# Performance work log

Hardware: AMD Instinct MI355X
Metric: run time of the kernel (lower is better)

The kernel has to match this reference:

```python
import jax, jax.numpy as jnp
import numpy as np

N = 100_000
E = 1_600_000
F_IN, D1, D2, D_EMB = 64, 32, 64, 64
NUM_GRAPHS = 16
BN_EPS = 1e-5


def _glorot(key, shape):
    fan_in, fan_out = shape[0], shape[1]
    lim = (6.0 / (fan_in + fan_out)) ** 0.5
    return jax.random.uniform(key, shape, jnp.float32, -lim, lim)


def setup_inputs() -> dict:
    key = jax.random.key(0)
    ks = jax.random.split(key, 12)
    x = jax.random.normal(ks[0], (N, F_IN), jnp.float32)
    edge_index = jax.random.randint(ks[1], (2, E), 0, N, jnp.int64)
    batch = jnp.sort(jax.random.randint(ks[2], (N,), 0, NUM_GRAPHS, jnp.int64))
    return {
        "x": x,
        "edge_index": edge_index,
        "batch": batch,
        "num_graphs": NUM_GRAPHS,
        "num_nodes": N,
        "W1a": _glorot(ks[3], (F_IN, D1)), "b1a": jnp.zeros((D1,), jnp.float32),
        "W1b": _glorot(ks[4], (D1, D2)), "b1b": jnp.zeros((D2,), jnp.float32),
        "g1": jnp.ones((D2,), jnp.float32), "be1": jnp.zeros((D2,), jnp.float32),
        "W2a": _glorot(ks[5], (D2, D2)), "b2a": jnp.zeros((D2,), jnp.float32),
        "W2b": _glorot(ks[6], (D2, D_EMB)), "b2b": jnp.zeros((D_EMB,), jnp.float32),
        "g2": jnp.ones((D_EMB,), jnp.float32), "be2": jnp.zeros((D_EMB,), jnp.float32),
    }


def _batchnorm_train(h, gamma, beta):
    mean = jnp.mean(h, axis=0)
    var = jnp.mean(jnp.square(h - mean), axis=0)  # biased var, as torch BN uses for normalization
    return (h - mean) * jax.lax.rsqrt(var + BN_EPS) * gamma + beta


def _gin_aggregate(x, src, dst, valid, n_nodes):
    # sum_{j in N(i)} x_j over valid edges only (masked scatter-add)
    msg = x[src] * valid[:, None]  # [E, D]
    return jax.ops.segment_sum(msg, dst, num_segments=n_nodes)


def reference(x, edge_index, batch, num_graphs, num_nodes,
              W1a, b1a, W1b, b1b, g1, be1,
              W2a, b2a, W2b, b2b, g2, be2):
    n_edges = edge_index.shape[1]
    per = n_edges // num_graphs
    # edge_mask: per-edge threshold g * num_nodes / num_graphs applied to both rows
    thresh = jnp.repeat(jnp.arange(num_graphs), per).astype(jnp.float32) * (num_nodes / num_graphs)
    valid = jnp.all(edge_index.astype(jnp.float32) - thresh[None, :] >= 0.0, axis=0)
    valid = valid.astype(x.dtype)
    src, dst = edge_index[0], edge_index[1]

    # GINConv 1 (eps=0): nn1(x + aggr)
    h = x + _gin_aggregate(x, src, dst, valid, num_nodes)
    h = jax.nn.relu(h @ W1a + b1a) @ W1b + b1b
    h = jax.nn.relu(h)
    h = _batchnorm_train(h, g1, be1)

    # GINConv 2
    h = h + _gin_aggregate(h, src, dst, valid, num_nodes)
    h = jax.nn.relu(h @ W2a + b2a) @ W2b + b2b
    h = jax.nn.relu(h)
    h = _batchnorm_train(h, g2, be2)

    # global_mean_pool
    sums = jax.ops.segment_sum(h, batch, num_segments=num_graphs)
    counts = jax.ops.segment_sum(jnp.ones((h.shape[0],), h.dtype), batch, num_segments=num_graphs)
    return sums / jnp.maximum(counts, 1.0)[:, None]
```

## Files before the change

kernel.cpp:

```cpp
#include <hip/hip_runtime.h>
#include <hip/hip_fp16.h>

#define NG 16
#define D 64
#define SLOT 32
#define NPB 128
#define INH 72

union HF4 { float4 f4; __half2 h2[4]; };
union HF2 { float2 f2; __half2 h2[2]; };

typedef _Float16 half4_t __attribute__((ext_vector_type(4)));
typedef float float4_t __attribute__((ext_vector_type(4)));

__device__ __forceinline__ float2 f2fma(float2 a, float2 b, float2 c) {
  return make_float2(fmaf(a.x, b.x, c.x), fmaf(a.y, b.y, c.y));
}

__device__ __forceinline__ void load16(const float4* __restrict__ feat4, int N,
                                       int q8, int4 a, int4 b, int4 c, int4 d,
                                       HF4* u) {
  int ix[16] = {a.x, a.y, a.z, a.w, b.x, b.y, b.z, b.w,
                c.x, c.y, c.z, c.w, d.x, d.y, d.z, d.w};
#pragma unroll
  for (int i = 0; i < 16; i++)
    u[i].f4 = feat4[(size_t)min(ix[i], N) * 8 + q8];
}

__device__ __forceinline__ void acc16(const HF4* u, float2* acc) {
#pragma unroll
  for (int i = 0; i < 16; i++) {
#pragma unroll
    for (int c = 0; c < 4; c++) {
      acc[c].x = fmaf(__low2float(u[i].h2[c]), 1.0f, acc[c].x);
      acc[c].y = fmaf(__high2float(u[i].h2[c]), 1.0f, acc[c].y);
    }
  }
}

__global__ void prep_kernel(const float* __restrict__ x,
                            float2* __restrict__ xh, int n4,
                            float4* __restrict__ xz, float4* __restrict__ hz,
                            const int* __restrict__ ei,
                            int* __restrict__ fill, int* __restrict__ col,
                            int E, int per, int tmul) {
  int t = blockIdx.x * 256 + threadIdx.x;
  if (blockIdx.x == 0 && threadIdx.x < 16) {
    float4 z = make_float4(0.f, 0.f, 0.f, 0.f);
    if (threadIdx.x < 8) xz[threadIdx.x] = z;
    else hz[threadIdx.x - 8] = z;
  }
  if (t < n4) {
    float4 v = ((const float4*)x)[t];
    HF2 u;
    u.h2[0] = __floats2half2_rn(v.x, v.y);
    u.h2[1] = __floats2half2_rn(v.z, v.w);
    xh[t] = u.f2;
  }
  if (t < E) {
    int src = ei[t];
    int dst = ei[E + t];
    int thr = (t / per) * tmul;
    if (src >= thr && dst >= thr) {
      int k = atomicAdd(&fill[dst], 1);
      if (k < SLOT) col[dst * SLOT + k] = src;
    }
  }
}

template <int MID, bool FOLD_BN, int EPI>
__global__ __launch_bounds__(512, 2) void fused_layer_kernel(
    const float4* __restrict__ feat4,
    const int* __restrict__ col, const int* __restrict__ deg,
    const float* __restrict__ bn_sum, const float* __restrict__ bn_sq,
    const float* __restrict__ bn_gamma, const float* __restrict__ bn_beta,
    float invN,
    const float* __restrict__ Wa, const float* __restrict__ ba,
    const float* __restrict__ Wb, const float* __restrict__ bb,
    float2* __restrict__ out2,
    const int* __restrict__ batch,
    float* __restrict__ st_sum,
    float* __restrict__ st_sq,
    float* __restrict__ cnt,
    int N) {
  constexpr int CT = MID / 16;

  __shared__ __align__(16) __half s_h[NPB * INH];
  __shared__ __align__(16) __half s_wa[MID * 64];
  __shared__ __align__(16) __half s_wb[64 * MID];
  __shared__ __align__(16) float s_ba[MID];
  __shared__ __align__(16) float s_bb[D];
  __shared__ float s_bna[FOLD_BN ? D : 1];
  __shared__ float s_bnb[FOLD_BN ? D : 1];
  __shared__ int s_cnt[2];

  int tid = threadIdx.x;
  int base = blockIdx.x * NPB;

  {
    constexpr int WA_SLOTS = MID * 16;
    constexpr int WB_SLOTS = MID * 16;
    for (int g = tid; g < WA_SLOTS + WB_SLOTS; g += 512) {
      half4_t v;
      if (g < WA_SLOTS) {
        int l = g & 63, kt = (g >> 6) & 3, ct = g >> 8;
        int k0 = kt * 16 + ((l >> 4) << 2);
        int c = ct * 16 + (l & 15);
#pragma unroll
        for (int i = 0; i < 4; i++) v[i] = (_Float16)Wa[(k0 + i) * MID + c];
        *(half4_t*)&s_wa[g * 4] = v;
      } else {
        int g2 = g - WA_SLOTS;
        int l = g2 & 63;
        int kt = (g2 >> 6) & (CT - 1);
        int ot = g2 >> (6 + (CT == 4 ? 2 : 1));
        int k0 = kt * 16 + ((l >> 4) << 2);
        int o = ot * 16 + (l & 15);
#pragma unroll
        for (int i = 0; i < 4; i++) v[i] = (_Float16)Wb[(k0 + i) * D + o];
        *(half4_t*)&s_wb[g2 * 4] = v;
      }
    }
  }
  if (tid < MID) s_ba[tid] = ba[tid];
  if (tid < D) s_bb[tid] = bb[tid];
  if (FOLD_BN && tid < D) {
    float mean = bn_sum[tid] * invN;
    float var = bn_sq[tid] * invN - mean * mean;
    float av = bn_gamma[tid] * rsqrtf(var + 1e-5f);
    s_bna[tid] = av;
    s_bnb[tid] = bn_beta[tid] - mean * av;
  }
  if (EPI == 2 && tid < 2) s_cnt[tid] = 0;
  __syncthreads();

  {
    int q8 = tid & 7;
#pragma unroll
    for (int s0 = 0; s0 < 2; s0++) {
      int slot = (tid >> 3) + 64 * s0;
      int node = base + slot;
      float2 acc[4];
      if (node < N) {
        int d = min(deg[node], SLOT);
        const int4* cp = (const int4*)(col + (size_t)node * SLOT);
        {
          HF4 s; s.f4 = feat4[(size_t)node * 8 + q8];
#pragma unroll
          for (int i = 0; i < 4; i++) acc[i] = __half22float2(s.h2[i]);
        }
        HF4 u[16];
        load16(feat4, N, q8, cp[0], cp[1], cp[2], cp[3], u);
        acc16(u, acc);
        if (__any(d > 16)) {
          load16(feat4, N, q8, cp[4], cp[5], cp[6], cp[7], u);
          acc16(u, acc);
        }
        if (FOLD_BN) {
          float dp = (float)(d + 1);
          int c0 = q8 * 8;
#pragma unroll
          for (int c = 0; c < 4; c++) {
            float2 a2 = *(const float2*)&s_bna[c0 + 2 * c];
            float2 b2 = *(const float2*)&s_bnb[c0 + 2 * c];
            acc[c] = f2fma(a2, acc[c], make_float2(dp * b2.x, dp * b2.y));
          }
        }
      } else {
#pragma unroll
        for (int i = 0; i < 4; i++) acc[i] = make_float2(0.f, 0.f);
      }
      HF4 o;
#pragma unroll
      for (int c = 0; c < 4; c++)
        o.h2[c] = __floats2half2_rn(acc[c].x, acc[c].y);
      *(float4*)&s_h[slot * INH + q8 * 8] = o.f4;
    }
  }
  __syncthreads();

  int w = tid >> 6;
  int l = tid & 63;
  int lg = l >> 4;
  int ln = l & 15;
  int nodeB = base + w * 16 + ln;

  half4_t hb[4];
#pragma unroll
  for (int kt = 0; kt < 4; kt++)
    hb[kt] = *(const half4_t*)&s_h[(w * 16 + ln) * INH + kt * 16 + lg * 4];

  float4_t c1[CT];
#pragma unroll
  for (int ct = 0; ct < CT; ct++) {
    c1[ct] = *(const float4_t*)&s_ba[ct * 16 + lg * 4];
#pragma unroll
    for (int kt = 0; kt < 4; kt++) {
      half4_t a = *(const half4_t*)&s_wa[((ct * 4 + kt) * 64 + l) * 4];
      c1[ct] = __builtin_amdgcn_mfma_f32_16x16x16f16(a, hb[kt], c1[ct], 0, 0, 0);
    }
  }
  half4_t mb[CT];
#pragma unroll
  for (int ct = 0; ct < CT; ct++) {
#pragma unroll
    for (int r = 0; r < 4; r++) mb[ct][r] = (_Float16)fmaxf(c1[ct][r], 0.f);
  }
  float4_t o4[4];
#pragma unroll
  for (int ot = 0; ot < 4; ot++) {
    o4[ot] = *(const float4_t*)&s_bb[ot * 16 + lg * 4];
#pragma unroll
    for (int kt = 0; kt < CT; kt++) {
      half4_t a = *(const half4_t*)&s_wb[((ot * CT + kt) * 64 + l) * 4];
      o4[ot] = __builtin_amdgcn_mfma_f32_16x16x16f16(a, mb[kt], o4[ot], 0, 0, 0);
    }
#pragma unroll
    for (int r = 0; r < 4; r++) o4[ot][r] = fmaxf(o4[ot][r], 0.f);
  }

  float* red = (float*)s_h;

  if (EPI == 1) {
    bool val = nodeB < N;
    if (val) {
#pragma unroll
      for (int ot = 0; ot < 4; ot++) {
        HF2 u;
        u.h2[0] = __floats2half2_rn(o4[ot][0], o4[ot][1]);
        u.h2[1] = __floats2half2_rn(o4[ot][2], o4[ot][3]);
        out2[(size_t)nodeB * 16 + ot * 4 + lg] = u.f2;
      }
    }
    float vm = val ? 1.f : 0.f;
#pragma unroll
    for (int ot = 0; ot < 4; ot++) {
      float4_t s, q;
#pragma unroll
      for (int r = 0; r < 4; r++) {
        float x = vm * o4[ot][r];
        s[r] = x; q[r] = x * o4[ot][r];
      }
#pragma unroll
      for (int m = 1; m < 16; m <<= 1) {
#pragma unroll
        for (int r = 0; r < 4; r++) {
          s[r] += __shfl_xor(s[r], m);
          q[r] += __shfl_xor(q[r], m);
        }
      }
      if (ln == 0) {
        *(float4_t*)&red[w * 576 + ot * 16 + lg * 4] = s;
        *(float4_t*)&red[w * 576 + 64 + ot * 16 + lg * 4] = q;
      }
    }
    __syncthreads();
    if (tid < D) {
      float s = 0.f, q = 0.f;
#pragma unroll
      for (int ww = 0; ww < 8; ww++) {
        s += red[ww * 576 + tid];
        q += red[ww * 576 + 64 + tid];
      }
      atomicAdd(&st_sum[tid], s);
      atomicAdd(&st_sq[tid], q);
    }
  }

  if (EPI == 2) {
    bool val = nodeB < N;
    int bl = val ? batch[nodeB] : -1;
    int g_lo = batch[base];
    int g_hi = batch[min(base + NPB - 1, N - 1)];
    float vm = val ? 1.f : 0.f;
    float wlo = (bl == g_lo) ? 1.f : 0.f;
    unsigned long long mlo = __ballot(lg == 0 && bl == g_lo);
    unsigned long long mhi = __ballot(lg == 0 && val && bl != g_lo);
    if (l == 0) {
      atomicAdd(&s_cnt[0], (int)__popcll(mlo));
      atomicAdd(&s_cnt[1], (int)__popcll(mhi));
    }
#pragma unroll
    for (int ot = 0; ot < 4; ot++) {
      float4_t sl, st, sq;
#pragma unroll
      for (int r = 0; r < 4; r++) {
        float x = vm * o4[ot][r];
        sl[r] = wlo * x;
        st[r] = x;
        sq[r] = x * o4[ot][r];
      }
#pragma unroll
      for (int m = 1; m < 16; m <<= 1) {
#pragma unroll
        for (int r = 0; r < 4; r++) {
          sl[r] += __shfl_xor(sl[r], m);
          st[r] += __shfl_xor(st[r], m);
          sq[r] += __shfl_xor(sq[r], m);
        }
      }
      if (ln == 0) {
        *(float4_t*)&red[w * 576 + ot * 16 + lg * 4] = sl;
        float4_t sh;
#pragma unroll
        for (int r = 0; r < 4; r++) sh[r] = st[r] - sl[r];
        *(float4_t*)&red[w * 576 + 64 + ot * 16 + lg * 4] = sh;
        *(float4_t*)&red[w * 576 + 128 + ot * 16 + lg * 4] = sq;
      }
    }
    __syncthreads();
    if (tid < D) {
      float sl = 0.f, sh = 0.f, sq = 0.f;
#pragma unroll
      for (int ww = 0; ww < 8; ww++) {
        sl += red[ww * 576 + tid];
        sh += red[ww * 576 + 64 + tid];
        sq += red[ww * 576 + 128 + tid];
      }
      atomicAdd(&st_sum[g_lo * D + tid], sl);
      if (g_hi != g_lo) atomicAdd(&st_sum[g_hi * D + tid], sh);
      atomicAdd(&st_sq[tid], sq);
    }
    if (tid == 0) {
      atomicAdd(&cnt[g_lo], (float)s_cnt[0]);
      if (g_hi != g_lo) atomicAdd(&cnt[g_hi], (float)s_cnt[1]);
    }
  }
}

__global__ void final_kernel(const float* __restrict__ pool,
                             const float* __restrict__ cnt,
                             const float* __restrict__ sq,
                             const float* __restrict__ gamma,
                             const float* __restrict__ beta,
                             float invN, float* __restrict__ out) {
  int c = threadIdx.x;
  float s = 0.f;
#pragma unroll
  for (int g = 0; g < NG; g++) s += pool[g * D + c];
  float mean = s * invN;
  float var = sq[c] * invN - mean * mean;
  float a = gamma[c] * rsqrtf(var + 1e-5f);
  float b = beta[c] - mean * a;
#pragma unroll
  for (int g = 0; g < NG; g++) {
    float n = cnt[g];
    out[g * D + c] = (a * pool[g * D + c] + n * b) / fmaxf(n, 1.f);
  }
}

extern "C" void kernel_launch(void* const* d_in, const int* in_sizes, int n_in,
                              void* d_out, int out_size, void* d_ws, size_t ws_size,
                              hipStream_t stream) {
  const float* x   = (const float*)d_in[0];
  const int* ei    = (const int*)d_in[1];
  const int* batch = (const int*)d_in[2];
  const float* W1a = (const float*)d_in[5];
  const float* b1a = (const float*)d_in[6];
  const float* W1b = (const float*)d_in[7];
  const float* b1b = (const float*)d_in[8];
  const float* g1  = (const float*)d_in[9];
  const float* be1 = (const float*)d_in[10];
  const float* W2a = (const float*)d_in[11];
  const float* b2a = (const float*)d_in[12];
  const float* W2b = (const float*)d_in[13];
  const float* b2b = (const float*)d_in[14];
  const float* g2  = (const float*)d_in[15];
  const float* be2 = (const float*)d_in[16];

  int N = in_sizes[0] / D;
  int E = in_sizes[1] / 2;
  int per = E / NG;
  int tmul = N / NG;
  float invN = 1.f / (float)N;

  float* ws = (float*)d_ws;
  size_t ndh = (size_t)(N + 1) * D / 2;
  float* h1h = ws;
  float* xh  = ws + ndh;
  int*   col = (int*)(ws + 2 * ndh);
  float* stats = ws + 2 * ndh + (size_t)N * SLOT;
  float* sum1 = stats;
  float* sq1  = stats + 64;
  float* pool = stats + 128;
  float* cnt  = stats + 128 + NG * D;
  float* sq2  = stats + 144 + NG * D;
  int*   fill = (int*)(stats + 208 + NG * D);

  hipMemsetAsync(stats, 0, (208 + NG * D + N) * sizeof(float), stream);
  hipMemsetAsync(col, 0x7F, (size_t)N * SLOT * sizeof(int), stream);

  int n4 = N * D / 4;
  int pgrid = (max(n4, E) + 255) / 256;
  prep_kernel<<<pgrid, 256, 0, stream>>>(
      x, (float2*)xh, n4,
      (float4*)(xh + (size_t)N * D / 2),
      (float4*)(h1h + (size_t)N * D / 2),
      ei, fill, col, E, per, tmul);

  int fblocks = (N + NPB - 1) / NPB;

  fused_layer_kernel<32, false, 1><<<fblocks, 512, 0, stream>>>(
      (const float4*)xh, col, fill, nullptr, nullptr, nullptr, nullptr, invN,
      W1a, b1a, W1b, b1b, (float2*)h1h, nullptr, sum1, sq1, nullptr, N);

  fused_layer_kernel<64, true, 2><<<fblocks, 512, 0, stream>>>(
      (const float4*)h1h, col, fill, sum1, sq1, g1, be1, invN,
      W2a, b2a, W2b, b2b, nullptr, batch, pool, sq2, cnt, N);

  final_kernel<<<1, 64, 0, stream>>>(pool, cnt, sq2, g2, be2, invN, (float*)d_out);
}
```

Measured before the change: 222.6 us.

## Sort nodes by degree within block and skip padded neighbor gathers in chunks

Each block builds a degree histogram and prefix scan in shared memory so the nodes of a block are processed in ascending-degree order. Wavefronts therefore see similar degrees, and neighbor gathers are issued in chunks of four that are skipped when no lane in the wave needs them. This replaces the old fixed 16-neighbor gather, which always loaded padded slots. It adds two extra barriers, shared atomics and a scan per block, and output rows are remapped through the permutation.

```diff
diff --git a/kernel.cpp b/kernel.cpp
--- a/kernel.cpp
+++ b/kernel.cpp
@@ -17,19 +17,16 @@
   return make_float2(fmaf(a.x, b.x, c.x), fmaf(a.y, b.y, c.y));
 }
 
-__device__ __forceinline__ void load16(const float4* __restrict__ feat4, int N,
-                                       int q8, int4 a, int4 b, int4 c, int4 d,
-                                       HF4* u) {
-  int ix[16] = {a.x, a.y, a.z, a.w, b.x, b.y, b.z, b.w,
-                c.x, c.y, c.z, c.w, d.x, d.y, d.z, d.w};
-#pragma unroll
-  for (int i = 0; i < 16; i++)
-    u[i].f4 = feat4[(size_t)min(ix[i], N) * 8 + q8];
-}
-
-__device__ __forceinline__ void acc16(const HF4* u, float2* acc) {
-#pragma unroll
-  for (int i = 0; i < 16; i++) {
+__device__ __forceinline__ void load4(const float4* __restrict__ feat4, int N,
+                                      int q8, int4 c, HF4* u) {
+  u[0].f4 = feat4[(size_t)min(c.x, N) * 8 + q8];
+  u[1].f4 = feat4[(size_t)min(c.y, N) * 8 + q8];
+  u[2].f4 = feat4[(size_t)min(c.z, N) * 8 + q8];
+  u[3].f4 = feat4[(size_t)min(c.w, N) * 8 + q8];
+}
+__device__ __forceinline__ void acc4(const HF4* u, float2* acc) {
+#pragma unroll
+  for (int i = 0; i < 4; i++) {
 #pragma unroll
     for (int c = 0; c < 4; c++) {
       acc[c].x = fmaf(__low2float(u[i].h2[c]), 1.0f, acc[c].x);
@@ -93,9 +90,38 @@
   __shared__ float s_bna[FOLD_BN ? D : 1];
   __shared__ float s_bnb[FOLD_BN ? D : 1];
   __shared__ int s_cnt[2];
+  __shared__ int s_pd[NPB];
+  __shared__ int s_hist[SLOT + 2];
 
   int tid = threadIdx.x;
   int base = blockIdx.x * NPB;
+
+  int ld = 0;
+  if (tid < NPB) {
+    int node = base + tid;
+    ld = (node < N) ? min(deg[node], SLOT) : 0;
+  }
+  if (tid >= NPB && tid < NPB + SLOT + 2) s_hist[tid - NPB] = 0;
+  if (EPI == 2 && tid < 2) s_cnt[tid] = 0;
+  __syncthreads();
+  if (tid < NPB) atomicAdd(&s_hist[ld], 1);
+  __syncthreads();
+  if (tid < 64) {
+    int b = tid;
+    int v = (b <= SLOT) ? s_hist[b] : 0;
+    int sum = v;
+#pragma unroll
+    for (int m = 1; m < 64; m <<= 1) {
+      int t2 = __shfl_up(sum, m, 64);
+      if (tid >= m) sum += t2;
+    }
+    if (b <= SLOT) s_hist[b] = sum - v;
+  }
+  __syncthreads();
+  if (tid < NPB) {
+    int k = atomicAdd(&s_hist[ld], 1);
+    s_pd[k] = tid | (ld << 8);
+  }
 
   {
     constexpr int WA_SLOTS = MID * 16;
@@ -131,7 +157,6 @@
     s_bna[tid] = av;
     s_bnb[tid] = bn_beta[tid] - mean * av;
   }
-  if (EPI == 2 && tid < 2) s_cnt[tid] = 0;
   __syncthreads();
 
   {
@@ -139,36 +164,54 @@
 #pragma unroll
     for (int s0 = 0; s0 < 2; s0++) {
       int slot = (tid >> 3) + 64 * s0;
-      int node = base + slot;
+      int pd = s_pd[slot];
+      int loc = pd & 255;
+      int d = pd >> 8;
+      int node = base + loc;
+      int an = min(node, N - 1);
+      const int4* cp = (const int4*)(col + (size_t)an * SLOT);
+      bool a0 = __any(d > 0), a1 = __any(d > 4);
+      bool a2 = __any(d > 8), a3 = __any(d > 12);
+      int4 c0, c1, c2, c3;
+      if (a0) c0 = cp[0];
+      if (a1) c1 = cp[1];
+      if (a2) c2 = cp[2];
+      if (a3) c3 = cp[3];
+      HF4 self; self.f4 = feat4[(size_t)min(node, N) * 8 + q8];
+      HF4 u[16];
+      if (a0) load4(feat4, N, q8, c0, u + 0);
+      if (a1) load4(feat4, N, q8, c1, u + 4);
+      if (a2) load4(feat4, N, q8, c2, u + 8);
+      if (a3) load4(feat4, N, q8, c3, u + 12);
       float2 acc[4];
-      if (node < N) {
-        int d = min(deg[node], SLOT);
-        const int4* cp = (const int4*)(col + (size_t)node * SLOT);
-        {
-          HF4 s; s.f4 = feat4[(size_t)node * 8 + q8];
-#pragma unroll
-          for (int i = 0; i < 4; i++) acc[i] = __half22float2(s.h2[i]);
+#pragma unroll
+      for (int c = 0; c < 4; c++) acc[c] = __half22float2(self.h2[c]);
+      if (a0) acc4(u + 0, acc);
+      if (a1) acc4(u + 4, acc);
+      if (a2) acc4(u + 8, acc);
+      if (a3) acc4(u + 12, acc);
+      if (__any(d > 16)) {
+        int4 c4 = cp[4], c5 = cp[5], c6 = cp[6], c7 = cp[7];
+        load4(feat4, N, q8, c4, u + 0);
+        load4(feat4, N, q8, c5, u + 4);
+        load4(feat4, N, q8, c6, u + 8);
+        load4(feat4, N, q8, c7, u + 12);
+        acc4(u + 0, acc); acc4(u + 4, acc);
+        acc4(u + 8, acc); acc4(u + 12, acc);
+      }
+      if (FOLD_BN) {
+        float dp = (float)(d + 1);
+        int c0f = q8 * 8;
+#pragma unroll
+        for (int c = 0; c < 4; c++) {
+          float2 a2f = *(const float2*)&s_bna[c0f + 2 * c];
+          float2 b2f = *(const float2*)&s_bnb[c0f + 2 * c];
+          acc[c] = f2fma(a2f, acc[c], make_float2(dp * b2f.x, dp * b2f.y));
         }
-        HF4 u[16];
-        load16(feat4, N, q8, cp[0], cp[1], cp[2], cp[3], u);
-        acc16(u, acc);
-        if (__any(d > 16)) {
-          load16(feat4, N, q8, cp[4], cp[5], cp[6], cp[7], u);
-          acc16(u, acc);
-        }
-        if (FOLD_BN) {
-          float dp = (float)(d + 1);
-          int c0 = q8 * 8;
-#pragma unroll
-          for (int c = 0; c < 4; c++) {
-            float2 a2 = *(const float2*)&s_bna[c0 + 2 * c];
-            float2 b2 = *(const float2*)&s_bnb[c0 + 2 * c];
-            acc[c] = f2fma(a2, acc[c], make_float2(dp * b2.x, dp * b2.y));
-          }
-        }
-      } else {
-#pragma unroll
-        for (int i = 0; i < 4; i++) acc[i] = make_float2(0.f, 0.f);
+      }
+      if (node >= N) {
+#pragma unroll
+        for (int c = 0; c < 4; c++) acc[c] = make_float2(0.f, 0.f);
       }
       HF4 o;
 #pragma unroll
@@ -183,7 +226,7 @@
   int l = tid & 63;
   int lg = l >> 4;
   int ln = l & 15;
-  int nodeB = base + w * 16 + ln;
+  int nodeB = base + (s_pd[w * 16 + ln] & 255);
 
   half4_t hb[4];
 #pragma unroll
```

Result: no change. 223.5 us (+0.4%).
